# Performance work log

Hardware: AMD Instinct MI355X
Metric: run time of the kernel (lower is better)

The kernel has to match this reference:

```python
import jax, jax.numpy as jnp
import numpy as np

B, C, W, H = 4, 256, 64, 64
CQK = C // 8  # 32


def setup_inputs() -> dict:
    key = jax.random.key(0)
    ks = jax.random.split(key, 8)
    scale = 0.02
    x = jax.random.normal(ks[0], (B, C, W, H), dtype=jnp.float32)
    wq = jax.random.normal(ks[1], (CQK, C), dtype=jnp.float32) * scale
    bq = jnp.zeros((CQK,), dtype=jnp.float32)
    wk = jax.random.normal(ks[2], (CQK, C), dtype=jnp.float32) * scale
    bk = jnp.zeros((CQK,), dtype=jnp.float32)
    wv = jax.random.normal(ks[3], (C, C), dtype=jnp.float32) * scale
    bv = jnp.zeros((C,), dtype=jnp.float32)
    gamma = jnp.zeros((1,), dtype=jnp.float32)
    return {"x": x, "wq": wq, "bq": bq, "wk": wk, "bk": bk,
            "wv": wv, "bv": bv, "gamma": gamma}


def reference(x, wq, bq, wk, bk, wv, bv, gamma):
    b, c, w, h = x.shape
    n = w * h
    xf = x.reshape(b, c, n)                         # b, C, N
    # 1x1 convs == channel matmuls
    q = jnp.einsum('oc,bcn->bno', wq, xf) + bq      # b, N, Cqk
    k = jnp.einsum('oc,bcn->bon', wk, xf) + bk[:, None]  # b, Cqk, N
    v = jnp.einsum('oc,bcn->bon', wv, xf) + bv[:, None]  # b, C, N
    energy = jnp.einsum('bic,bcj->bij', q, k)       # b, N, N
    attention = jax.nn.softmax(energy, axis=-1)     # b, N, N
    # out[b,c,i] = sum_j v[b,c,j] * attention[b,i,j]
    out = jnp.einsum('bcj,bij->bci', v, attention)  # b, C, N
    out = out.reshape(b, c, w, h)
    out = gamma[0] * out + x
    return out, attention
```

## Files before the change

kernel.cpp:

```cpp
#include <hip/hip_runtime.h>

#define NB 4
#define NC 256
#define NN 4096
#define NQK 32

typedef short short4v __attribute__((ext_vector_type(4)));
typedef short short8 __attribute__((ext_vector_type(8)));
typedef float f32x4 __attribute__((ext_vector_type(4)));
typedef float f32x16 __attribute__((ext_vector_type(16)));

#define MFMA16(a, b, c) __builtin_amdgcn_mfma_f32_16x16x32_bf16((a), (b), (c), 0, 0, 0)
#define MFMA32(a, b, c) __builtin_amdgcn_mfma_f32_32x32x16_bf16((a), (b), (c), 0, 0, 0)

#if __has_builtin(__builtin_amdgcn_exp2f)
#define EXP2(x) __builtin_amdgcn_exp2f(x)
#else
#define EXP2(x) __expf((x) * 0.6931471805599453f)
#endif

#define L2E 1.4426950408889634f

__device__ __forceinline__ unsigned short f2bf(float f) {
  unsigned int u = __builtin_bit_cast(unsigned int, f);
  u += 0x7fffu + ((u >> 16) & 1u);
  return (unsigned short)(u >> 16);
}

__global__ void k_prep(const float* __restrict__ wq, const float* __restrict__ wk,
                       const float* __restrict__ wv,
                       unsigned short* __restrict__ wqb, unsigned short* __restrict__ wkb,
                       unsigned short* __restrict__ wvb) {
  int i = blockIdx.x * 256 + threadIdx.x;
  if (i < NQK * NC) { wqb[i] = f2bf(wq[i]); wkb[i] = f2bf(wk[i]); }
  wvb[i] = f2bf(wv[i]);
}

__global__ __launch_bounds__(256) void k_proj(
    const float* __restrict__ x,
    const unsigned short* __restrict__ wqb, const unsigned short* __restrict__ wkb,
    const unsigned short* __restrict__ wvb,
    const float* __restrict__ bq, const float* __restrict__ bk,
    const float* __restrict__ bv,
    unsigned short* __restrict__ qb, unsigned short* __restrict__ kTb,
    unsigned short* __restrict__ vb) {
  __shared__ unsigned short ldsx[32][264];
  __shared__ unsigned short ldsvt[256][40];
  int b = blockIdx.y, n0 = blockIdx.x * 32;
  int t = threadIdx.x, w = t >> 6, l = t & 63, lm = l & 15, lk = l >> 4;
  const float* xb = x + (size_t)b * NC * NN + n0;
#pragma unroll
  for (int p = 0; p < 8; ++p) {
    int c = p * 32 + (t >> 3);
    int n4 = (t & 7) * 4;
    f32x4 v4 = *(const f32x4*)(xb + (size_t)c * NN + n4);
#pragma unroll
    for (int u = 0; u < 4; ++u) ldsx[n4 + u][c] = f2bf(v4[u]);
  }
  __syncthreads();
  int s = w & 1, h = w >> 1;
  f32x4 qa[2] = {}, ka[2] = {}, va[10] = {};
  if (h == 0) {
#pragma unroll
    for (int kk = 0; kk < 8; ++kk) {
      short8 a = *(const short8*)(&ldsx[s * 16 + lm][kk * 32 + lk * 8]);
      const unsigned short* wqp = wqb + lm * NC + kk * 32 + lk * 8;
      const unsigned short* wkp = wkb + lm * NC + kk * 32 + lk * 8;
      qa[0] = MFMA16(a, *(const short8*)(wqp), qa[0]);
      qa[1] = MFMA16(a, *(const short8*)(wqp + 16 * NC), qa[1]);
      ka[0] = MFMA16(a, *(const short8*)(wkp), ka[0]);
      ka[1] = MFMA16(a, *(const short8*)(wkp + 16 * NC), ka[1]);
#pragma unroll
      for (int j = 0; j < 6; ++j) {
        const unsigned short* wvp = wvb + (size_t)(j * 16 + lm) * NC + kk * 32 + lk * 8;
        va[j] = MFMA16(a, *(const short8*)(wvp), va[j]);
      }
    }
  } else {
#pragma unroll
    for (int kk = 0; kk < 8; ++kk) {
      short8 a = *(const short8*)(&ldsx[s * 16 + lm][kk * 32 + lk * 8]);
#pragma unroll
      for (int j = 0; j < 10; ++j) {
        const unsigned short* wvp = wvb + (size_t)(96 + j * 16 + lm) * NC + kk * 32 + lk * 8;
        va[j] = MFMA16(a, *(const short8*)(wvp), va[j]);
      }
    }
  }
  if (h == 0) {
    int nrow = n0 + s * 16 + lk * 4;
#pragma unroll
    for (int f = 0; f < 2; ++f) {
      float bqv = bq[f * 16 + lm], bkv = bk[f * 16 + lm];
#pragma unroll
      for (int r = 0; r < 4; ++r) {
        size_t o = ((size_t)(b * NN + nrow + r)) * NQK + f * 16 + lm;
        qb[o] = f2bf((qa[f][r] + bqv) * L2E);
        kTb[o] = f2bf(ka[f][r] + bkv);
      }
    }
#pragma unroll
    for (int j = 0; j < 6; ++j) {
      float bvv = bv[j * 16 + lm];
#pragma unroll
      for (int r = 0; r < 4; ++r)
        ldsvt[j * 16 + lm][s * 16 + lk * 4 + r] = f2bf(va[j][r] + bvv);
    }
  } else {
#pragma unroll
    for (int j = 0; j < 10; ++j) {
      float bvv = bv[96 + j * 16 + lm];
#pragma unroll
      for (int r = 0; r < 4; ++r)
        ldsvt[96 + j * 16 + lm][s * 16 + lk * 4 + r] = f2bf(va[j][r] + bvv);
    }
  }
  __syncthreads();
#pragma unroll
  for (int p = 0; p < 4; ++p) {
    int c = p * 64 + (t >> 2);
    int np = (t & 3) * 8;
    *(short8*)(vb + ((size_t)(b * NC + c)) * NN + n0 + np) =
        *(const short8*)(&ldsvt[c][np]);
  }
}

__global__ __launch_bounds__(512) void k_attn(
    const unsigned short* __restrict__ qb, const unsigned short* __restrict__ kTb,
    const unsigned short* __restrict__ vb, const float* __restrict__ x,
    const float* __restrict__ gamma, float* __restrict__ out,
    float* __restrict__ attn) {
  __shared__ unsigned short ldsv[256 * 64];
  __shared__ unsigned short ldsp[2][64 * 64];
  __shared__ float ldsd[64][8];
  int id = blockIdx.x;
  int b = (id >> 1) & 3;
  int i0 = (((id >> 3) << 1) | (id & 1)) * 64;
  int t = threadIdx.x, w = t >> 6, l = t & 63, lm = l & 15, lk = l >> 4;
  const f32x4 z = {0.f, 0.f, 0.f, 0.f};

  const unsigned short* qbb = qb + ((size_t)(b * NN + i0 + lm)) * NQK + lk * 8;
  short8 qa0 = *(const short8*)(qbb);
  short8 qa1 = *(const short8*)(qbb + 16 * NQK);
  short8 qa2 = *(const short8*)(qbb + 32 * NQK);
  short8 qa3 = *(const short8*)(qbb + 48 * NQK);
  const unsigned short* kbase = kTb + (size_t)b * NN * NQK + lk * 8;

  float s0 = 0.f, s1 = 0.f, s2 = 0.f, s3 = 0.f;
  for (int j0 = w * 512; j0 < w * 512 + 512; j0 += 16) {
    short8 kf = *(const short8*)(kbase + (size_t)(j0 + lm) * NQK);
    f32x4 e0 = MFMA16(kf, qa0, z);
    f32x4 e1 = MFMA16(kf, qa1, z);
    f32x4 e2 = MFMA16(kf, qa2, z);
    f32x4 e3 = MFMA16(kf, qa3, z);
#pragma unroll
    for (int r = 0; r < 4; ++r) {
      s0 += EXP2(e0[r]); s1 += EXP2(e1[r]);
      s2 += EXP2(e2[r]); s3 += EXP2(e3[r]);
    }
  }
  s0 += __shfl_xor(s0, 16); s0 += __shfl_xor(s0, 32);
  s1 += __shfl_xor(s1, 16); s1 += __shfl_xor(s1, 32);
  s2 += __shfl_xor(s2, 16); s2 += __shfl_xor(s2, 32);
  s3 += __shfl_xor(s3, 16); s3 += __shfl_xor(s3, 32);
  if (lk == 0) {
    ldsd[lm][w] = s0;       ldsd[16 + lm][w] = s1;
    ldsd[32 + lm][w] = s2;  ldsd[48 + lm][w] = s3;
  }
  __syncthreads();

  int is = w & 3, jh = w >> 2;
  int cg = w;
  short8 qe = (is == 0) ? qa0 : (is == 1) ? qa1 : (is == 2) ? qa2 : qa3;
  int prow = is * 16 + lm;
  f32x4 dA = *(const f32x4*)(&ldsd[prow][0]);
  f32x4 dB = *(const f32x4*)(&ldsd[prow][4]);
  float dinv = 1.0f / (dA[0] + dA[1] + dA[2] + dA[3] + dB[0] + dB[1] + dB[2] + dB[3]);

  float g = gamma[0];
  float* attn_b = attn + (size_t)b * NN * NN;
  float* aptr = attn_b + (size_t)(i0 + prow) * NN + jh * 32 + lk * 4;
  const unsigned short* vbb = vb + (size_t)b * NC * NN;
  int vrow = t >> 3, vcol = t & 7;
  int vx = (vcol * 16) ^ ((vrow & 7) << 4);
  char* vbase = (char*)ldsv;
  int pc0 = (jh * 64 + lk * 8) ^ ((prow & 7) << 4);
  int pc1 = (jh * 64 + lk * 8 + 32) ^ ((prow & 7) << 4);
  int rowa = cg * 32 + (l & 31);
  int xa = (rowa & 7) << 4;
  int xp = ((l & 31) & 7) << 4;
  int chalf = (l >> 5) * 16;
  int rp0 = (l & 31) * 128, rp1 = (32 + (l & 31)) * 128;

  short8 vr0 = *(const short8*)(vbb + (size_t)(vrow) * NN + vcol * 8);
  short8 vr1 = *(const short8*)(vbb + (size_t)(64 + vrow) * NN + vcol * 8);
  short8 vr2 = *(const short8*)(vbb + (size_t)(128 + vrow) * NN + vcol * 8);
  short8 vr3 = *(const short8*)(vbb + (size_t)(192 + vrow) * NN + vcol * 8);

  f32x16 acc0 = {}, acc1 = {};
  for (int tt = 0; tt < 64; ++tt) {
    int p = tt & 1;
    int j0 = tt * 64;
    int jb = j0 + jh * 32;
    short8 kf0 = *(const short8*)(kbase + (size_t)(jb + lm) * NQK);
    short8 kf1 = *(const short8*)(kbase + (size_t)(jb + 16 + lm) * NQK);
    f32x4 e0 = MFMA16(kf0, qe, z);
    f32x4 e1 = MFMA16(kf1, qe, z);
    f32x4 p0, p1;
#pragma unroll
    for (int r = 0; r < 4; ++r) {
      p0[r] = EXP2(e0[r]) * dinv;
      p1[r] = EXP2(e1[r]) * dinv;
    }
    __builtin_nontemporal_store(p0, (f32x4*)(aptr + j0));
    __builtin_nontemporal_store(p1, (f32x4*)(aptr + j0 + 16));
    short4v pb0, pb1;
#pragma unroll
    for (int r = 0; r < 4; ++r) {
      pb0[r] = (short)f2bf(p0[r]);
      pb1[r] = (short)f2bf(p1[r]);
    }
    char* pb = (char*)(&ldsp[p][0]) + prow * 128;
    *(short4v*)(pb + pc0) = pb0;
    *(short4v*)(pb + pc1) = pb1;
    __syncthreads();
    *(short8*)(vbase + (vrow) * 128 + vx) = vr0;
    *(short8*)(vbase + (64 + vrow) * 128 + vx) = vr1;
    *(short8*)(vbase + (128 + vrow) * 128 + vx) = vr2;
    *(short8*)(vbase + (192 + vrow) * 128 + vx) = vr3;
    {
      size_t jn = (size_t)(((tt + 1) & 63) * 64);
      vr0 = *(const short8*)(vbb + (size_t)(vrow) * NN + jn + vcol * 8);
      vr1 = *(const short8*)(vbb + (size_t)(64 + vrow) * NN + jn + vcol * 8);
      vr2 = *(const short8*)(vbb + (size_t)(128 + vrow) * NN + jn + vcol * 8);
      vr3 = *(const short8*)(vbb + (size_t)(192 + vrow) * NN + jn + vcol * 8);
    }
    __syncthreads();
    const char* pvp = (const char*)(&ldsp[p][0]);
    const char* abase = vbase + rowa * 128;
    __builtin_amdgcn_s_setprio(1);
#pragma unroll
    for (int kk = 0; kk < 4; ++kk) {
      int cb = kk * 32 + chalf;
      short8 af = *(const short8*)(abase + (cb ^ xa));
      short8 pf0 = *(const short8*)(pvp + rp0 + (cb ^ xp));
      short8 pf1 = *(const short8*)(pvp + rp1 + (cb ^ xp));
      acc0 = MFMA32(af, pf0, acc0);
      acc1 = MFMA32(af, pf1, acc1);
    }
    __builtin_amdgcn_s_setprio(0);
  }

  int ieg0 = i0 + (l & 31), ieg1 = i0 + 32 + (l & 31);
  int crb = cg * 32 + 4 * (l >> 5);
#pragma unroll
  for (int reg = 0; reg < 16; ++reg) {
    int c = crb + (reg & 3) + 8 * (reg >> 2);
    size_t o0 = ((size_t)(b * NC + c)) * NN + ieg0;
    size_t o1 = ((size_t)(b * NC + c)) * NN + ieg1;
    out[o0] = g * acc0[reg] + x[o0];
    out[o1] = g * acc1[reg] + x[o1];
  }
}

extern "C" void kernel_launch(void* const* d_in, const int* in_sizes, int n_in,
                              void* d_out, int out_size, void* d_ws, size_t ws_size,
                              hipStream_t stream) {
  (void)in_sizes; (void)n_in; (void)out_size; (void)ws_size;
  const float* x  = (const float*)d_in[0];
  const float* wq = (const float*)d_in[1];
  const float* bq = (const float*)d_in[2];
  const float* wk = (const float*)d_in[3];
  const float* bk = (const float*)d_in[4];
  const float* wv = (const float*)d_in[5];
  const float* bv = (const float*)d_in[6];
  const float* gamma = (const float*)d_in[7];
  float* out  = (float*)d_out;
  float* attn = out + (size_t)NB * NC * NN;

  char* ws = (char*)d_ws;
  unsigned short* qb  = (unsigned short*)(ws);
  unsigned short* kTb = (unsigned short*)(ws + 1048576);
  unsigned short* vb  = (unsigned short*)(ws + 2097152);
  unsigned short* wqb = (unsigned short*)(ws + 10485760);
  unsigned short* wkb = (unsigned short*)(ws + 10502144);
  unsigned short* wvb = (unsigned short*)(ws + 10518528);

  k_prep<<<dim3(256), dim3(256), 0, stream>>>(wq, wk, wv, wqb, wkb, wvb);
  k_proj<<<dim3(128, 4), dim3(256), 0, stream>>>(x, wqb, wkb, wvb, bq, bk, bv,
                                                 qb, kTb, vb);
  k_attn<<<dim3(256), dim3(512), 0, stream>>>(qb, kTb, vb, x, gamma, out, attn);
}
```

Baseline: 374.0 us.

## Halve attention row tile to 32 and run two 256-thread blocks per CU

The attention kernel now handles 32 query rows per block with 4 waves instead of 64 rows with 8 waves. The grid doubles to 512 blocks, with launch bounds set for two resident blocks per CU so the two blocks' barriers are independent. Each wave now owns 64 output channels across 32 rows, and the XOR swizzle for the V tile moves from the LDS write address to the global read column. The trade-off is that each V tile is loaded and staged once per 32 rows instead of once per 64, doubling V traffic and LDS writes per output row.

Result: no change. 370.3 us (-1.0%).

```diff
diff --git a/kernel.cpp b/kernel.cpp
--- a/kernel.cpp
+++ b/kernel.cpp
@@ -125,83 +125,70 @@
   }
 }
 
-__global__ __launch_bounds__(512) void k_attn(
+__global__ __launch_bounds__(256, 2) void k_attn(
     const unsigned short* __restrict__ qb, const unsigned short* __restrict__ kTb,
     const unsigned short* __restrict__ vb, const float* __restrict__ x,
     const float* __restrict__ gamma, float* __restrict__ out,
     float* __restrict__ attn) {
   __shared__ unsigned short ldsv[256 * 64];
-  __shared__ unsigned short ldsp[2][64 * 64];
-  __shared__ float ldsd[64][8];
+  __shared__ unsigned short ldsp[2][32 * 64];
+  __shared__ float ldsd[32][4];
   int id = blockIdx.x;
-  int b = (id >> 1) & 3;
-  int i0 = (((id >> 3) << 1) | (id & 1)) * 64;
+  int xcd = id & 7;
+  int b = xcd >> 1;
+  int i0 = (((id >> 3) << 1) | (xcd & 1)) * 32;
   int t = threadIdx.x, w = t >> 6, l = t & 63, lm = l & 15, lk = l >> 4;
   const f32x4 z = {0.f, 0.f, 0.f, 0.f};
 
   const unsigned short* qbb = qb + ((size_t)(b * NN + i0 + lm)) * NQK + lk * 8;
   short8 qa0 = *(const short8*)(qbb);
   short8 qa1 = *(const short8*)(qbb + 16 * NQK);
-  short8 qa2 = *(const short8*)(qbb + 32 * NQK);
-  short8 qa3 = *(const short8*)(qbb + 48 * NQK);
   const unsigned short* kbase = kTb + (size_t)b * NN * NQK + lk * 8;
 
-  float s0 = 0.f, s1 = 0.f, s2 = 0.f, s3 = 0.f;
-  for (int j0 = w * 512; j0 < w * 512 + 512; j0 += 16) {
+  float s0 = 0.f, s1 = 0.f;
+  for (int j0 = w * 1024; j0 < w * 1024 + 1024; j0 += 16) {
     short8 kf = *(const short8*)(kbase + (size_t)(j0 + lm) * NQK);
     f32x4 e0 = MFMA16(kf, qa0, z);
     f32x4 e1 = MFMA16(kf, qa1, z);
-    f32x4 e2 = MFMA16(kf, qa2, z);
-    f32x4 e3 = MFMA16(kf, qa3, z);
-#pragma unroll
-    for (int r = 0; r < 4; ++r) {
-      s0 += EXP2(e0[r]); s1 += EXP2(e1[r]);
-      s2 += EXP2(e2[r]); s3 += EXP2(e3[r]);
-    }
+#pragma unroll
+    for (int r = 0; r < 4; ++r) { s0 += EXP2(e0[r]); s1 += EXP2(e1[r]); }
   }
   s0 += __shfl_xor(s0, 16); s0 += __shfl_xor(s0, 32);
   s1 += __shfl_xor(s1, 16); s1 += __shfl_xor(s1, 32);
-  s2 += __shfl_xor(s2, 16); s2 += __shfl_xor(s2, 32);
-  s3 += __shfl_xor(s3, 16); s3 += __shfl_xor(s3, 32);
-  if (lk == 0) {
-    ldsd[lm][w] = s0;       ldsd[16 + lm][w] = s1;
-    ldsd[32 + lm][w] = s2;  ldsd[48 + lm][w] = s3;
-  }
+  if (lk == 0) { ldsd[lm][w] = s0; ldsd[16 + lm][w] = s1; }
   __syncthreads();
 
-  int is = w & 3, jh = w >> 2;
-  int cg = w;
-  short8 qe = (is == 0) ? qa0 : (is == 1) ? qa1 : (is == 2) ? qa2 : qa3;
+  int is = w & 1, jh = w >> 1;
+  short8 qe = is ? qa1 : qa0;
   int prow = is * 16 + lm;
-  f32x4 dA = *(const f32x4*)(&ldsd[prow][0]);
-  f32x4 dB = *(const f32x4*)(&ldsd[prow][4]);
-  float dinv = 1.0f / (dA[0] + dA[1] + dA[2] + dA[3] + dB[0] + dB[1] + dB[2] + dB[3]);
+  f32x4 d4 = *(const f32x4*)(&ldsd[prow][0]);
+  float dinv = 1.0f / (d4[0] + d4[1] + d4[2] + d4[3]);
 
   float g = gamma[0];
   float* attn_b = attn + (size_t)b * NN * NN;
   float* aptr = attn_b + (size_t)(i0 + prow) * NN + jh * 32 + lk * 4;
   const unsigned short* vbb = vb + (size_t)b * NC * NN;
   int vrow = t >> 3, vcol = t & 7;
-  int vx = (vcol * 16) ^ ((vrow & 7) << 4);
+  int voff = ((vcol * 16) ^ ((vrow & 7) << 4)) >> 1;
   char* vbase = (char*)ldsv;
-  int pc0 = (jh * 64 + lk * 8) ^ ((prow & 7) << 4);
-  int pc1 = (jh * 64 + lk * 8 + 32) ^ ((prow & 7) << 4);
-  int rowa = cg * 32 + (l & 31);
-  int xa = (rowa & 7) << 4;
-  int xp = ((l & 31) & 7) << 4;
-  int chalf = (l >> 5) * 16;
-  int rp0 = (l & 31) * 128, rp1 = (32 + (l & 31)) * 128;
-
-  short8 vr0 = *(const short8*)(vbb + (size_t)(vrow) * NN + vcol * 8);
-  short8 vr1 = *(const short8*)(vbb + (size_t)(64 + vrow) * NN + vcol * 8);
-  short8 vr2 = *(const short8*)(vbb + (size_t)(128 + vrow) * NN + vcol * 8);
-  short8 vr3 = *(const short8*)(vbb + (size_t)(192 + vrow) * NN + vcol * 8);
+  int psw = (prow & 7) << 4;
+  int pc0 = (jh * 64 + lk * 8) ^ psw;
+  int pc1 = (jh * 64 + lk * 8 + 32) ^ psw;
+  int rowa = w * 64 + (l & 31);
+  int sa = (rowa & 7) << 4;
+  int sp = ((l & 31) & 7) << 4;
+  int khalf = (l >> 5) * 16;
+  const char* abase = vbase + rowa * 128;
+
+  short8 vr[8];
+#pragma unroll
+  for (int s = 0; s < 8; ++s)
+    vr[s] = *(const short8*)(vbb + (size_t)(vrow + 32 * s) * NN + voff);
 
   f32x16 acc0 = {}, acc1 = {};
   for (int tt = 0; tt < 64; ++tt) {
     int p = tt & 1;
-    int j0 = tt * 64;
-    int jb = j0 + jh * 32;
+    int jb = tt * 64 + jh * 32;
     short8 kf0 = *(const short8*)(kbase + (size_t)(jb + lm) * NQK);
     short8 kf1 = *(const short8*)(kbase + (size_t)(jb + 16 + lm) * NQK);
     f32x4 e0 = MFMA16(kf0, qe, z);
@@ -212,8 +199,8 @@
       p0[r] = EXP2(e0[r]) * dinv;
       p1[r] = EXP2(e1[r]) * dinv;
     }
-    __builtin_nontemporal_store(p0, (f32x4*)(aptr + j0));
-    __builtin_nontemporal_store(p1, (f32x4*)(aptr + j0 + 16));
+    __builtin_nontemporal_store(p0, (f32x4*)(aptr + tt * 64));
+    __builtin_nontemporal_store(p1, (f32x4*)(aptr + tt * 64 + 16));
     short4v pb0, pb1;
 #pragma unroll
     for (int r = 0; r < 4; ++r) {
@@ -224,40 +211,37 @@
     *(short4v*)(pb + pc0) = pb0;
     *(short4v*)(pb + pc1) = pb1;
     __syncthreads();
-    *(short8*)(vbase + (vrow) * 128 + vx) = vr0;
-    *(short8*)(vbase + (64 + vrow) * 128 + vx) = vr1;
-    *(short8*)(vbase + (128 + vrow) * 128 + vx) = vr2;
-    *(short8*)(vbase + (192 + vrow) * 128 + vx) = vr3;
+#pragma unroll
+    for (int s = 0; s < 8; ++s)
+      *(short8*)(vbase + (vrow + 32 * s) * 128 + vcol * 16) = vr[s];
     {
       size_t jn = (size_t)(((tt + 1) & 63) * 64);
-      vr0 = *(const short8*)(vbb + (size_t)(vrow) * NN + jn + vcol * 8);
-      vr1 = *(const short8*)(vbb + (size_t)(64 + vrow) * NN + jn + vcol * 8);
-      vr2 = *(const short8*)(vbb + (size_t)(128 + vrow) * NN + jn + vcol * 8);
-      vr3 = *(const short8*)(vbb + (size_t)(192 + vrow) * NN + jn + vcol * 8);
+#pragma unroll
+      for (int s = 0; s < 8; ++s)
+        vr[s] = *(const short8*)(vbb + (size_t)(vrow + 32 * s) * NN + jn + voff);
     }
     __syncthreads();
-    const char* pvp = (const char*)(&ldsp[p][0]);
-    const char* abase = vbase + rowa * 128;
+    const char* pvp = (const char*)(&ldsp[p][0]) + (l & 31) * 128;
     __builtin_amdgcn_s_setprio(1);
 #pragma unroll
     for (int kk = 0; kk < 4; ++kk) {
-      int cb = kk * 32 + chalf;
-      short8 af = *(const short8*)(abase + (cb ^ xa));
-      short8 pf0 = *(const short8*)(pvp + rp0 + (cb ^ xp));
-      short8 pf1 = *(const short8*)(pvp + rp1 + (cb ^ xp));
-      acc0 = MFMA32(af, pf0, acc0);
-      acc1 = MFMA32(af, pf1, acc1);
+      int cb = kk * 32 + khalf;
+      short8 af0 = *(const short8*)(abase + (cb ^ sa));
+      short8 af1 = *(const short8*)(abase + 32 * 128 + (cb ^ sa));
+      short8 pf = *(const short8*)(pvp + (cb ^ sp));
+      acc0 = MFMA32(af0, pf, acc0);
+      acc1 = MFMA32(af1, pf, acc1);
     }
     __builtin_amdgcn_s_setprio(0);
   }
 
-  int ieg0 = i0 + (l & 31), ieg1 = i0 + 32 + (l & 31);
-  int crb = cg * 32 + 4 * (l >> 5);
+  int ieg = i0 + (l & 31);
+  int crb = w * 64 + 4 * (l >> 5);
 #pragma unroll
   for (int reg = 0; reg < 16; ++reg) {
     int c = crb + (reg & 3) + 8 * (reg >> 2);
-    size_t o0 = ((size_t)(b * NC + c)) * NN + ieg0;
-    size_t o1 = ((size_t)(b * NC + c)) * NN + ieg1;
+    size_t o0 = ((size_t)(b * NC + c)) * NN + ieg;
+    size_t o1 = ((size_t)(b * NC + c + 32)) * NN + ieg;
     out[o0] = g * acc0[reg] + x[o0];
     out[o1] = g * acc1[reg] + x[o1];
   }
@@ -289,5 +273,5 @@
   k_prep<<<dim3(256), dim3(256), 0, stream>>>(wq, wk, wv, wqb, wkb, wvb);
   k_proj<<<dim3(128, 4), dim3(256), 0, stream>>>(x, wqb, wkb, wvb, bq, bk, bv,
                                                  qb, kTb, vb);
-  k_attn<<<dim3(256), dim3(512), 0, stream>>>(qb, kTb, vb, x, gamma, out, attn);
-}
+  k_attn<<<dim3(512), dim3(256), 0, stream>>>(qb, kTb, vb, x, gamma, out, attn);
+}
```
